# Kernel optimization log

Measured on AMD Instinct MI355X. Metric: run time of the kernel, lower is better.

The kernel has to match this reference:

```python
import jax, jax.numpy as jnp
import numpy as np

N_NODES = 100000
N_EDGES = 3200000
NFEAT = 256
NHID = 256


def setup_inputs() -> dict:
    key = jax.random.key(0)
    k_x, k_ws, k_wn, k_src, k_dst = jax.random.split(key, 5)
    x = jax.random.normal(k_x, (N_NODES, NFEAT), dtype=jnp.float32)
    W_self = jax.random.normal(k_ws, (NFEAT, NHID), dtype=jnp.float32) * (1.0 / np.sqrt(NFEAT))
    W_neigh = jax.random.normal(k_wn, (NFEAT, NHID), dtype=jnp.float32) * (1.0 / np.sqrt(NFEAT))
    b = jnp.zeros((NHID,), dtype=jnp.float32)
    edge_src = jax.random.randint(k_src, (N_EDGES,), 0, N_NODES, dtype=jnp.int32)
    edge_dst = jax.random.randint(k_dst, (N_EDGES,), 0, N_NODES, dtype=jnp.int32)
    return {"x": x, "W_self": W_self, "W_neigh": W_neigh, "b": b,
            "edge_src": edge_src, "edge_dst": edge_dst}


def reference(x, W_self, W_neigh, b, edge_src, edge_dst):
    n = x.shape[0]
    # mean aggregation over incoming edges: gather src feats, scatter-add to dst
    msg = x[edge_src]                                              # [E, F]
    agg = jax.ops.segment_sum(msg, edge_dst, num_segments=n)       # [N, F]
    deg = jax.ops.segment_sum(jnp.ones_like(edge_dst, dtype=x.dtype),
                              edge_dst, num_segments=n)            # [N]
    h_neigh = agg / jnp.maximum(deg, 1.0)[:, None]                 # mean (0 for isolated)
    # SAGEConv 'mean': fc_self(x) + fc_neigh(h_neigh) (bias on neigh branch)
    out = x @ W_self + h_neigh @ W_neigh + b                       # [N, H]
    return jax.nn.relu(out)
```

## Files before the change

kernel.cpp:

```cpp
#include <hip/hip_runtime.h>
#include <stdint.h>

typedef __attribute__((ext_vector_type(8))) short bf16x8;
typedef __attribute__((ext_vector_type(4))) float f32x4;
typedef __attribute__((ext_vector_type(2))) float f32x2;

#define NF 256
#define NH 256
#define KTOT 512
#define BM 128
#define BN 128
#define BK 32
#define LDP 40
#define EB 256
#define NBIN 512

static __device__ __forceinline__ float bf2f(unsigned short u){
  union { unsigned int i; float f; } v; v.i = ((unsigned int)u) << 16; return v.f;
}
static __device__ __forceinline__ unsigned short f2bf(float f){
  union { float f; unsigned int u; } v; v.f = f;
  unsigned int r = v.u + 0x7fffu + ((v.u >> 16) & 1u);
  return (unsigned short)(r >> 16);
}
static __device__ __forceinline__ unsigned int f2e4(float f){
  union { float f; unsigned int u; } v; v.f = f;
  unsigned int s = v.u >> 31;
  unsigned int mag = v.u & 0x7fffffffu;
  if (mag > 0x43E00000u) mag = 0x43E00000u;
  unsigned int r = mag + 0x7ffffu + ((mag >> 20) & 1u);
  if (r < 0x3C800000u) return 0u;
  return (s << 7) | (((r >> 20) - 960u) & 0x7fu);
}

__global__ void k_cvt_xq(const float* __restrict__ x, unsigned int* __restrict__ xq, int n8){
  for (int i = blockIdx.x*blockDim.x + threadIdx.x; i < n8; i += gridDim.x*blockDim.x){
    const float4* p = (const float4*)(x + (size_t)i*8);
    float4 a = p[0], b = p[1];
    unsigned int w0 = f2e4(a.x) | (f2e4(a.y)<<8) | (f2e4(a.z)<<16) | (f2e4(a.w)<<24);
    unsigned int w1 = f2e4(b.x) | (f2e4(b.y)<<8) | (f2e4(b.z)<<16) | (f2e4(b.w)<<24);
    uint2 o; o.x = w0; o.y = w1;
    ((uint2*)xq)[i] = o;
  }
}

__global__ void k_cvt_w(const float* __restrict__ Ws, const float* __restrict__ Wn,
                        unsigned short* __restrict__ Wt){
  int t = blockIdx.x*blockDim.x + threadIdx.x;
  if (t >= NH*KTOT) return;
  int n = t >> 9, k = t & 511;
  float v = (k < NF) ? Ws[(size_t)k*NH + n] : Wn[(size_t)(k-NF)*NH + n];
  Wt[t] = (unsigned short)f2bf(v);
}

__global__ void __launch_bounds__(256) k_bhist(const int* __restrict__ dst,
                                               int* __restrict__ H, int ne){
  __shared__ int lh[NBIN];
  int blk = blockIdx.x, t = threadIdx.x;
  for (int i = t; i < NBIN; i += 256) lh[i] = 0;
  __syncthreads();
  int chunk = (ne + EB - 1) / EB;
  int e0 = blk * chunk, e1 = ne < e0 + chunk ? ne : e0 + chunk;
  for (int e = e0 + t; e < e1; e += 256)
    atomicAdd(&lh[((unsigned)dst[e]) >> 8], 1);
  __syncthreads();
  for (int i = t; i < NBIN; i += 256) H[i*EB + blk] = lh[i];
}

__global__ void k_partial(const int* __restrict__ deg, int* __restrict__ partial, int n){
  __shared__ int sm[256];
  int b = blockIdx.x, t = threadIdx.x;
  int i0 = b*1024 + t*4;
  int s = 0;
  if (i0 + 3 < n){ int4 v = *(const int4*)(deg + i0); s = v.x+v.y+v.z+v.w; }
  else { for (int j=0;j<4;j++) if (i0+j < n) s += deg[i0+j]; }
  sm[t] = s; __syncthreads();
  for (int d = 128; d > 0; d >>= 1){ if (t < d) sm[t] += sm[t+d]; __syncthreads(); }
  if (t == 0) partial[b] = sm[0];
}

__global__ void k_scanp(int* __restrict__ partial, int nb){
  __shared__ int sm[128];
  int t = threadIdx.x;
  int v = (t < nb) ? partial[t] : 0;
  sm[t] = v; __syncthreads();
  for (int d = 1; d < 128; d <<= 1){
    int u = (t >= d) ? sm[t-d] : 0; __syncthreads();
    sm[t] += u; __syncthreads();
  }
  if (t < nb) partial[t] = sm[t] - v;
}

__global__ void k_scanapply(const int* __restrict__ deg, const int* __restrict__ partial,
                            int* __restrict__ off, int n, int ne){
  __shared__ int sm[256];
  int b = blockIdx.x, t = threadIdx.x;
  int i0 = b*1024 + t*4;
  int d0=0,d1=0,d2=0,d3=0;
  if (i0 + 3 < n){ int4 v = *(const int4*)(deg + i0); d0=v.x; d1=v.y; d2=v.z; d3=v.w; }
  else { if(i0<n)d0=deg[i0]; if(i0+1<n)d1=deg[i0+1]; if(i0+2<n)d2=deg[i0+2]; if(i0+3<n)d3=deg[i0+3]; }
  int s = d0+d1+d2+d3;
  sm[t] = s; __syncthreads();
  for (int d = 1; d < 256; d <<= 1){
    int u = (t >= d) ? sm[t-d] : 0; __syncthreads();
    sm[t] += u; __syncthreads();
  }
  int run = partial[b] + sm[t] - s;
  if (i0   < n) off[i0]   = run; run += d0;
  if (i0+1 < n) off[i0+1] = run; run += d1;
  if (i0+2 < n) off[i0+2] = run; run += d2;
  if (i0+3 < n) off[i0+3] = run;
  if (b == 0 && t == 0) off[n] = ne;
}

__global__ void __launch_bounds__(256) k_bscat(const int* __restrict__ src,
                                               const int* __restrict__ dst,
                                               const int* __restrict__ base,
                                               unsigned int* __restrict__ bkt, int ne){
  __shared__ int lc[NBIN];
  __shared__ int lb[NBIN];
  int blk = blockIdx.x, t = threadIdx.x;
  for (int i = t; i < NBIN; i += 256){ lc[i] = 0; lb[i] = base[i*EB + blk]; }
  __syncthreads();
  int chunk = (ne + EB - 1) / EB;
  int e0 = blk * chunk, e1 = ne < e0 + chunk ? ne : e0 + chunk;
  for (int e = e0 + t; e < e1; e += 256){
    int d = dst[e];
    int bin = ((unsigned)d) >> 8;
    int p = lb[bin] + atomicAdd(&lc[bin], 1);
    bkt[p] = (((unsigned)src[e]) << 8) | ((unsigned)d & 255u);
  }
}

__global__ void __launch_bounds__(256) k_csr(const unsigned int* __restrict__ bkt,
                                             const int* __restrict__ base,
                                             int* __restrict__ off, int* __restrict__ col,
                                             int nn, int ne){
  __shared__ int lh[256], sc[256], se[256], lc[256];
  int b = blockIdx.x, t = threadIdx.x;
  int n0 = base[b*EB], n1 = base[(b+1)*EB];
  lh[t] = 0; lc[t] = 0;
  __syncthreads();
  for (int e = n0 + t; e < n1; e += 256)
    atomicAdd(&lh[bkt[e] & 255u], 1);
  __syncthreads();
  int v = lh[t];
  sc[t] = v; __syncthreads();
  for (int d = 1; d < 256; d <<= 1){
    int u = (t >= d) ? sc[t-d] : 0; __syncthreads();
    sc[t] += u; __syncthreads();
  }
  int excl = sc[t] - v;
  se[t] = excl;
  int node = b*256 + t;
  if (node <= nn) off[node] = n0 + excl;
  __syncthreads();
  for (int e = n0 + t; e < n1; e += 256){
    unsigned u = bkt[e];
    int low = (int)(u & 255u);
    int r = atomicAdd(&lc[low], 1);
    col[n0 + se[low] + r] = (int)(u >> 8);
  }
}

static __device__ __forceinline__ void acc4(unsigned int v, float& a0, float& a1, float& a2, float& a3){
#if __has_builtin(__builtin_amdgcn_cvt_pk_f32_fp8)
  f32x2 lo = __builtin_amdgcn_cvt_pk_f32_fp8((int)v, false);
  f32x2 hi = __builtin_amdgcn_cvt_pk_f32_fp8((int)v, true);
  a0 += lo[0]; a1 += lo[1]; a2 += hi[0]; a3 += hi[1];
#else
  #pragma unroll
  for (int j = 0; j < 4; j++){
    unsigned int b = (v >> (8*j)) & 0xffu;
    unsigned int tt = b & 0x7fu;
    union { unsigned int u; float f; } w;
    w.u = ((tt + 960u) << 20) | ((b & 0x80u) << 24);
    float f = tt ? w.f : 0.f;
    if (j==0) a0 += f; else if (j==1) a1 += f; else if (j==2) a2 += f; else a3 += f;
  }
#endif
}

__global__ void __launch_bounds__(256) k_agg(const unsigned char* __restrict__ xq,
                                             const int* __restrict__ off,
                                             const int* __restrict__ col,
                                             unsigned short* __restrict__ hb, int n){
  int w = threadIdx.x >> 6;
  int lane = threadIdx.x & 63;
  int node = blockIdx.x*4 + w;
  if (node >= n) return;
  int e0 = off[node], e1 = off[node+1];
  float a0=0.f, a1=0.f, a2=0.f, a3=0.f;
  int e = e0;
  for (; e + 3 < e1; e += 4){
    int s0 = col[e], s1 = col[e+1], s2 = col[e+2], s3 = col[e+3];
    unsigned int v0 = ((const unsigned int*)(xq + (size_t)s0*NF))[lane];
    unsigned int v1 = ((const unsigned int*)(xq + (size_t)s1*NF))[lane];
    unsigned int v2 = ((const unsigned int*)(xq + (size_t)s2*NF))[lane];
    unsigned int v3 = ((const unsigned int*)(xq + (size_t)s3*NF))[lane];
    acc4(v0, a0,a1,a2,a3);
    acc4(v1, a0,a1,a2,a3);
    acc4(v2, a0,a1,a2,a3);
    acc4(v3, a0,a1,a2,a3);
  }
  for (; e < e1; e++){
    int s0 = col[e];
    unsigned int v0 = ((const unsigned int*)(xq + (size_t)s0*NF))[lane];
    acc4(v0, a0,a1,a2,a3);
  }
  float inv = 1.f / (float)((e1 - e0) > 1 ? (e1 - e0) : 1);
  ushort4 o;
  o.x = f2bf(a0*inv); o.y = f2bf(a1*inv); o.z = f2bf(a2*inv); o.w = f2bf(a3*inv);
  ((ushort4*)(hb + (size_t)node*NF))[lane] = o;
}

__global__ void __launch_bounds__(256) k_gemm(const float* __restrict__ xf,
                                              const unsigned short* __restrict__ hb,
                                              const unsigned short* __restrict__ Wt,
                                              const float* __restrict__ bias,
                                              float* __restrict__ out, int M){
  __shared__ unsigned short As[BM*LDP];
  __shared__ unsigned short Bs[BN*LDP];
  int t = threadIdx.x;
  int m0 = blockIdx.x * BM;
  int n0 = blockIdx.y * BN;
  int w = t >> 6, lane = t & 63;
  int wm = w >> 1, wn = w & 1;
  int lrow = lane & 15, k8 = (lane >> 4) * 8;

  f32x4 acc[4][4];
  #pragma unroll
  for (int i=0;i<4;i++)
    #pragma unroll
    for (int j=0;j<4;j++) acc[i][j] = (f32x4){0.f,0.f,0.f,0.f};

  for (int kk = 0; kk < KTOT; kk += BK){
    __syncthreads();
    if (kk < NF){
      #pragma unroll
      for (int p = 0; p < 2; p++){
        int f = p*256 + t;
        int r = f >> 2, c = (f & 3) * 8;
        int gr = m0 + r; if (gr > M-1) gr = M-1;
        const float* src = xf + (size_t)gr*NF + kk + c;
        float4 u0 = *(const float4*)src;
        float4 u1 = *(const float4*)(src + 4);
        ushort4 o0, o1;
        o0.x=f2bf(u0.x); o0.y=f2bf(u0.y); o0.z=f2bf(u0.z); o0.w=f2bf(u0.w);
        o1.x=f2bf(u1.x); o1.y=f2bf(u1.y); o1.z=f2bf(u1.z); o1.w=f2bf(u1.w);
        *(ushort4*)(&As[r*LDP + c])     = o0;
        *(ushort4*)(&As[r*LDP + c + 4]) = o1;
      }
    } else {
      const unsigned short* Asrc = hb + (kk - NF);
      #pragma unroll
      for (int p = 0; p < 2; p++){
        int f = p*256 + t;
        int r = f >> 2, c = (f & 3) * 8;
        int gr = m0 + r; if (gr > M-1) gr = M-1;
        int4 v = *(const int4*)(Asrc + (size_t)gr*NF + c);
        *(int4*)(&As[r*LDP + c]) = v;
      }
    }
    #pragma unroll
    for (int p = 0; p < 2; p++){
      int f = p*256 + t;
      int r = f >> 2, c = (f & 3) * 8;
      int4 v = *(const int4*)(Wt + (size_t)(n0 + r)*KTOT + kk + c);
      *(int4*)(&Bs[r*LDP + c]) = v;
    }
    __syncthreads();
    bf16x8 af[4], bfr[4];
    #pragma unroll
    for (int mi=0;mi<4;mi++)
      af[mi] = *(const bf16x8*)(&As[(wm*64 + mi*16 + lrow)*LDP + k8]);
    #pragma unroll
    for (int ni=0;ni<4;ni++)
      bfr[ni] = *(const bf16x8*)(&Bs[(wn*64 + ni*16 + lrow)*LDP + k8]);
    #pragma unroll
    for (int mi=0;mi<4;mi++)
      #pragma unroll
      for (int ni=0;ni<4;ni++)
        acc[mi][ni] = __builtin_amdgcn_mfma_f32_16x16x32_bf16(af[mi], bfr[ni], acc[mi][ni], 0, 0, 0);
  }

  #pragma unroll
  for (int ni=0;ni<4;ni++){
    int cn = n0 + wn*64 + ni*16 + lrow;
    float bv = bias[cn];
    #pragma unroll
    for (int mi=0;mi<4;mi++){
      #pragma unroll
      for (int r=0;r<4;r++){
        int rm = m0 + wm*64 + mi*16 + (lane>>4)*4 + r;
        if (rm < M){
          float v = acc[mi][ni][r] + bv;
          out[(size_t)rm*NH + cn] = v > 0.f ? v : 0.f;
        }
      }
    }
  }
}

extern "C" void kernel_launch(void* const* d_in, const int* in_sizes, int n_in,
                              void* d_out, int out_size, void* d_ws, size_t ws_size,
                              hipStream_t stream){
  const float* x      = (const float*)d_in[0];
  const float* Wself  = (const float*)d_in[1];
  const float* Wneigh = (const float*)d_in[2];
  const float* bias   = (const float*)d_in[3];
  const int*   esrc   = (const int*)d_in[4];
  const int*   edst   = (const int*)d_in[5];
  const int nn = in_sizes[0] / NF;
  const int ne = in_sizes[4];

  char* w = (char*)d_ws;
  auto alloc = [&](size_t bytes)->char*{
    char* p = w; w += (bytes + 511) & ~size_t(511); return p;
  };
  unsigned char*  xq  = (unsigned char*)alloc((size_t)nn*NF);
  unsigned short* hb  = (unsigned short*)alloc((size_t)nn*NF*2);
  unsigned int* bkt   = (unsigned int*)alloc((size_t)ne*4);
  int* col            = (int*)alloc((size_t)ne*4);
  int* H              = (int*)alloc((size_t)(NBIN*EB + 1)*4);
  int* base           = (int*)alloc((size_t)(NBIN*EB + 1)*4);
  int* off            = (int*)alloc((size_t)(nn+1)*4);
  unsigned short* Wt  = (unsigned short*)alloc((size_t)NH*KTOT*2);
  int* partial        = (int*)alloc(4096);

  const int nH = NBIN*EB;
  const int nb = nH / 1024;

  k_cvt_xq<<<2048, 256, 0, stream>>>(x, (unsigned int*)xq, nn*NF/8);
  k_cvt_w<<<(NH*KTOT + 255)/256, 256, 0, stream>>>(Wself, Wneigh, Wt);
  k_bhist<<<EB, 256, 0, stream>>>(edst, H, ne);
  k_partial<<<nb, 256, 0, stream>>>(H, partial, nH);
  k_scanp<<<1, 128, 0, stream>>>(partial, nb);
  k_scanapply<<<nb, 256, 0, stream>>>(H, partial, base, nH, ne);
  k_bscat<<<EB, 256, 0, stream>>>(esrc, edst, base, bkt, ne);
  k_csr<<<NBIN, 256, 0, stream>>>(bkt, base, off, col, nn, ne);
  k_agg<<<(nn + 3)/4, 256, 0, stream>>>(xq, off, col, hb, nn);
  dim3 gg((nn + BM - 1)/BM, NH/BN);
  k_gemm<<<gg, 256, 0, stream>>>(x, hb, Wt, bias, (float*)d_out, nn);
}
```

Before: 350.8 us.

## Store aggregated features as fp8, batch edge indices via readlane, widen GEMM K-tile

The aggregation kernel now loads up to 64 column indices per wavefront in one coalesced read and broadcasts them with readlane. It also unrolls 8 gathers in flight and writes the mean as fp8 instead of bf16, which halves the intermediate buffer. The GEMM decodes the fp8 neighbor features to bf16 while staging into LDS, and its K tile doubles to 64 so there are half as many barrier iterations. The aim is to cut memory traffic and index-load latency, at the cost of extra precision loss from the fp8 intermediate and more LDS per block.

```diff
diff --git a/kernel.cpp b/kernel.cpp
--- a/kernel.cpp
+++ b/kernel.cpp
@@ -10,14 +10,11 @@
 #define KTOT 512
 #define BM 128
 #define BN 128
-#define BK 32
-#define LDP 40
+#define BK2 64
+#define LDP2 72
 #define EB 256
 #define NBIN 512
 
-static __device__ __forceinline__ float bf2f(unsigned short u){
-  union { unsigned int i; float f; } v; v.i = ((unsigned int)u) << 16; return v.f;
-}
 static __device__ __forceinline__ unsigned short f2bf(float f){
   union { float f; unsigned int u; } v; v.f = f;
   unsigned int r = v.u + 0x7fffu + ((v.u >> 16) & 1u);
@@ -180,47 +177,83 @@
   }
 #endif
 }
-
-__global__ void __launch_bounds__(256) k_agg(const unsigned char* __restrict__ xq,
+static __device__ __forceinline__ ushort4 dec8(unsigned int v){
+#if __has_builtin(__builtin_amdgcn_cvt_pk_f32_fp8)
+  f32x2 lo = __builtin_amdgcn_cvt_pk_f32_fp8((int)v, false);
+  f32x2 hi = __builtin_amdgcn_cvt_pk_f32_fp8((int)v, true);
+  ushort4 o; o.x=f2bf(lo[0]); o.y=f2bf(lo[1]); o.z=f2bf(hi[0]); o.w=f2bf(hi[1]);
+  return o;
+#else
+  ushort4 o; unsigned short r[4];
+  #pragma unroll
+  for (int j = 0; j < 4; j++){
+    unsigned int b = (v >> (8*j)) & 0xffu;
+    unsigned int tt = b & 0x7fu;
+    union { unsigned int u; float f; } w;
+    w.u = ((tt + 960u) << 20) | ((b & 0x80u) << 24);
+    r[j] = tt ? f2bf(w.f) : (unsigned short)0;
+  }
+  o.x=r[0]; o.y=r[1]; o.z=r[2]; o.w=r[3];
+  return o;
+#endif
+}
+
+__global__ void __launch_bounds__(256) k_agg(const unsigned int* __restrict__ xw,
                                              const int* __restrict__ off,
                                              const int* __restrict__ col,
-                                             unsigned short* __restrict__ hb, int n){
+                                             unsigned int* __restrict__ hq, int n){
   int w = threadIdx.x >> 6;
   int lane = threadIdx.x & 63;
   int node = blockIdx.x*4 + w;
   if (node >= n) return;
   int e0 = off[node], e1 = off[node+1];
+  int deg = e1 - e0;
   float a0=0.f, a1=0.f, a2=0.f, a3=0.f;
-  int e = e0;
-  for (; e + 3 < e1; e += 4){
-    int s0 = col[e], s1 = col[e+1], s2 = col[e+2], s3 = col[e+3];
-    unsigned int v0 = ((const unsigned int*)(xq + (size_t)s0*NF))[lane];
-    unsigned int v1 = ((const unsigned int*)(xq + (size_t)s1*NF))[lane];
-    unsigned int v2 = ((const unsigned int*)(xq + (size_t)s2*NF))[lane];
-    unsigned int v3 = ((const unsigned int*)(xq + (size_t)s3*NF))[lane];
-    acc4(v0, a0,a1,a2,a3);
-    acc4(v1, a0,a1,a2,a3);
-    acc4(v2, a0,a1,a2,a3);
-    acc4(v3, a0,a1,a2,a3);
-  }
-  for (; e < e1; e++){
-    int s0 = col[e];
-    unsigned int v0 = ((const unsigned int*)(xq + (size_t)s0*NF))[lane];
-    acc4(v0, a0,a1,a2,a3);
-  }
-  float inv = 1.f / (float)((e1 - e0) > 1 ? (e1 - e0) : 1);
-  ushort4 o;
-  o.x = f2bf(a0*inv); o.y = f2bf(a1*inv); o.z = f2bf(a2*inv); o.w = f2bf(a3*inv);
-  ((ushort4*)(hb + (size_t)node*NF))[lane] = o;
+  for (int c0 = 0; c0 < deg; c0 += 64){
+    int len = deg - c0; if (len > 64) len = 64;
+    int cv = 0;
+    if (lane < len) cv = col[e0 + c0 + lane];
+    int i = 0;
+    for (; i + 8 <= len; i += 8){
+      int s0 = __builtin_amdgcn_readlane(cv, i+0);
+      int s1 = __builtin_amdgcn_readlane(cv, i+1);
+      int s2 = __builtin_amdgcn_readlane(cv, i+2);
+      int s3 = __builtin_amdgcn_readlane(cv, i+3);
+      int s4 = __builtin_amdgcn_readlane(cv, i+4);
+      int s5 = __builtin_amdgcn_readlane(cv, i+5);
+      int s6 = __builtin_amdgcn_readlane(cv, i+6);
+      int s7 = __builtin_amdgcn_readlane(cv, i+7);
+      unsigned int u0 = xw[(size_t)s0*64 + lane];
+      unsigned int u1 = xw[(size_t)s1*64 + lane];
+      unsigned int u2 = xw[(size_t)s2*64 + lane];
+      unsigned int u3 = xw[(size_t)s3*64 + lane];
+      unsigned int u4 = xw[(size_t)s4*64 + lane];
+      unsigned int u5 = xw[(size_t)s5*64 + lane];
+      unsigned int u6 = xw[(size_t)s6*64 + lane];
+      unsigned int u7 = xw[(size_t)s7*64 + lane];
+      acc4(u0,a0,a1,a2,a3); acc4(u1,a0,a1,a2,a3);
+      acc4(u2,a0,a1,a2,a3); acc4(u3,a0,a1,a2,a3);
+      acc4(u4,a0,a1,a2,a3); acc4(u5,a0,a1,a2,a3);
+      acc4(u6,a0,a1,a2,a3); acc4(u7,a0,a1,a2,a3);
+    }
+    for (; i < len; ++i){
+      int s = __builtin_amdgcn_readlane(cv, i);
+      unsigned int u = xw[(size_t)s*64 + lane];
+      acc4(u,a0,a1,a2,a3);
+    }
+  }
+  float inv = 1.f / (float)(deg > 1 ? deg : 1);
+  unsigned int o = f2e4(a0*inv) | (f2e4(a1*inv)<<8) | (f2e4(a2*inv)<<16) | (f2e4(a3*inv)<<24);
+  hq[(size_t)node*64 + lane] = o;
 }
 
 __global__ void __launch_bounds__(256) k_gemm(const float* __restrict__ xf,
-                                              const unsigned short* __restrict__ hb,
+                                              const unsigned char* __restrict__ hq,
                                               const unsigned short* __restrict__ Wt,
                                               const float* __restrict__ bias,
                                               float* __restrict__ out, int M){
-  __shared__ unsigned short As[BM*LDP];
-  __shared__ unsigned short Bs[BN*LDP];
+  __shared__ unsigned short As[BM*LDP2];
+  __shared__ unsigned short Bs[BN*LDP2];
   int t = threadIdx.x;
   int m0 = blockIdx.x * BM;
   int n0 = blockIdx.y * BN;
@@ -234,54 +267,57 @@
     #pragma unroll
     for (int j=0;j<4;j++) acc[i][j] = (f32x4){0.f,0.f,0.f,0.f};
 
-  for (int kk = 0; kk < KTOT; kk += BK){
+  for (int kk = 0; kk < KTOT; kk += BK2){
     __syncthreads();
     if (kk < NF){
       #pragma unroll
-      for (int p = 0; p < 2; p++){
-        int f = p*256 + t;
-        int r = f >> 2, c = (f & 3) * 8;
+      for (int q = 0; q < 4; q++){
+        int chunk = q*256 + t;
+        int r = chunk >> 3, c8 = (chunk & 7) * 8;
         int gr = m0 + r; if (gr > M-1) gr = M-1;
-        const float* src = xf + (size_t)gr*NF + kk + c;
-        float4 u0 = *(const float4*)src;
-        float4 u1 = *(const float4*)(src + 4);
+        const float* src = xf + (size_t)gr*NF + kk + c8;
+        float4 u0 = ((const float4*)src)[0];
+        float4 u1 = ((const float4*)src)[1];
         ushort4 o0, o1;
         o0.x=f2bf(u0.x); o0.y=f2bf(u0.y); o0.z=f2bf(u0.z); o0.w=f2bf(u0.w);
         o1.x=f2bf(u1.x); o1.y=f2bf(u1.y); o1.z=f2bf(u1.z); o1.w=f2bf(u1.w);
-        *(ushort4*)(&As[r*LDP + c])     = o0;
-        *(ushort4*)(&As[r*LDP + c + 4]) = o1;
+        *(ushort4*)(&As[r*LDP2 + c8])     = o0;
+        *(ushort4*)(&As[r*LDP2 + c8 + 4]) = o1;
       }
     } else {
-      const unsigned short* Asrc = hb + (kk - NF);
-      #pragma unroll
-      for (int p = 0; p < 2; p++){
-        int f = p*256 + t;
-        int r = f >> 2, c = (f & 3) * 8;
+      #pragma unroll
+      for (int q = 0; q < 4; q++){
+        int chunk = q*256 + t;
+        int r = chunk >> 3, c8 = (chunk & 7) * 8;
         int gr = m0 + r; if (gr > M-1) gr = M-1;
-        int4 v = *(const int4*)(Asrc + (size_t)gr*NF + c);
-        *(int4*)(&As[r*LDP + c]) = v;
+        uint2 v = *(const uint2*)(hq + (size_t)gr*NF + (kk - NF) + c8);
+        *(ushort4*)(&As[r*LDP2 + c8])     = dec8(v.x);
+        *(ushort4*)(&As[r*LDP2 + c8 + 4]) = dec8(v.y);
       }
     }
     #pragma unroll
-    for (int p = 0; p < 2; p++){
-      int f = p*256 + t;
-      int r = f >> 2, c = (f & 3) * 8;
-      int4 v = *(const int4*)(Wt + (size_t)(n0 + r)*KTOT + kk + c);
-      *(int4*)(&Bs[r*LDP + c]) = v;
+    for (int q = 0; q < 4; q++){
+      int chunk = q*256 + t;
+      int r = chunk >> 3, c8 = (chunk & 7) * 8;
+      int4 v = *(const int4*)(Wt + (size_t)(n0 + r)*KTOT + kk + c8);
+      *(int4*)(&Bs[r*LDP2 + c8]) = v;
     }
     __syncthreads();
-    bf16x8 af[4], bfr[4];
     #pragma unroll
-    for (int mi=0;mi<4;mi++)
-      af[mi] = *(const bf16x8*)(&As[(wm*64 + mi*16 + lrow)*LDP + k8]);
-    #pragma unroll
-    for (int ni=0;ni<4;ni++)
-      bfr[ni] = *(const bf16x8*)(&Bs[(wn*64 + ni*16 + lrow)*LDP + k8]);
-    #pragma unroll
-    for (int mi=0;mi<4;mi++)
+    for (int ks = 0; ks < 2; ks++){
+      bf16x8 af[4], bfr[4];
+      #pragma unroll
+      for (int mi=0;mi<4;mi++)
+        af[mi] = *(const bf16x8*)(&As[(wm*64 + mi*16 + lrow)*LDP2 + ks*32 + k8]);
       #pragma unroll
       for (int ni=0;ni<4;ni++)
-        acc[mi][ni] = __builtin_amdgcn_mfma_f32_16x16x32_bf16(af[mi], bfr[ni], acc[mi][ni], 0, 0, 0);
+        bfr[ni] = *(const bf16x8*)(&Bs[(wn*64 + ni*16 + lrow)*LDP2 + ks*32 + k8]);
+      #pragma unroll
+      for (int mi=0;mi<4;mi++)
+        #pragma unroll
+        for (int ni=0;ni<4;ni++)
+          acc[mi][ni] = __builtin_amdgcn_mfma_f32_16x16x32_bf16(af[mi], bfr[ni], acc[mi][ni], 0, 0, 0);
+    }
   }
 
   #pragma unroll
@@ -319,7 +355,7 @@
     char* p = w; w += (bytes + 511) & ~size_t(511); return p;
   };
   unsigned char*  xq  = (unsigned char*)alloc((size_t)nn*NF);
-  unsigned short* hb  = (unsigned short*)alloc((size_t)nn*NF*2);
+  unsigned char*  hq  = (unsigned char*)alloc((size_t)nn*NF);
   unsigned int* bkt   = (unsigned int*)alloc((size_t)ne*4);
   int* col            = (int*)alloc((size_t)ne*4);
   int* H              = (int*)alloc((size_t)(NBIN*EB + 1)*4);
@@ -339,7 +375,7 @@
   k_scanapply<<<nb, 256, 0, stream>>>(H, partial, base, nH, ne);
   k_bscat<<<EB, 256, 0, stream>>>(esrc, edst, base, bkt, ne);
   k_csr<<<NBIN, 256, 0, stream>>>(bkt, base, off, col, nn, ne);
-  k_agg<<<(nn + 3)/4, 256, 0, stream>>>(xq, off, col, hb, nn);
+  k_agg<<<(nn + 3)/4, 256, 0, stream>>>((const unsigned int*)xq, off, col, (unsigned int*)hq, nn);
   dim3 gg((nn + BM - 1)/BM, NH/BN);
-  k_gemm<<<gg, 256, 0, stream>>>(x, hb, Wt, bias, (float*)d_out, nn);
-}
+  k_gemm<<<gg, 256, 0, stream>>>(x, hq, Wt, bias, (float*)d_out, nn);
+}
```

Measured after the change: 340.8 us. -2.8%, faster.
